# Kernel tuning notes

Hardware: AMD Instinct MI355X
Metric: run time of the kernel (lower is better)

The kernel has to match this reference:

```python
import jax, jax.numpy as jnp
import numpy as np

D_MODEL = 1024
SLOTS = 4096
LEVELS = 3
B, T = 4, 4096
TOP_K = 8  # k = min(8, slots)


def setup_inputs() -> dict:
    key = jax.random.key(0)
    ks = jax.random.split(key, 8)
    # xavier-uniform-ish scale for K/V
    lim_kv = np.sqrt(6.0 / (SLOTS + D_MODEL)).astype(np.float32)
    lim_w1 = np.sqrt(6.0 / (D_MODEL + D_MODEL // 2)).astype(np.float32)
    lim_w2 = np.sqrt(6.0 / (D_MODEL // 2 + LEVELS)).astype(np.float32)
    return {
        "q": jax.random.normal(ks[0], (B, T, D_MODEL), dtype=jnp.float32),
        "Ks": jax.random.uniform(ks[1], (LEVELS, SLOTS, D_MODEL), jnp.float32, -lim_kv, lim_kv),
        "Vs": jax.random.uniform(ks[2], (LEVELS, SLOTS, D_MODEL), jnp.float32, -lim_kv, lim_kv),
        "saliences": jnp.zeros((LEVELS, SLOTS), dtype=jnp.float32),
        "router_W1": jax.random.uniform(ks[3], (D_MODEL, D_MODEL // 2), jnp.float32, -lim_w1, lim_w1),
        "router_b1": jnp.zeros((D_MODEL // 2,), dtype=jnp.float32),
        "router_W2": jax.random.uniform(ks[4], (D_MODEL // 2, LEVELS), jnp.float32, -lim_w2, lim_w2),
        "router_b2": jnp.zeros((LEVELS,), dtype=jnp.float32),
    }


def reference(q, Ks, Vs, saliences, router_W1, router_b1, router_W2, router_b2):
    Bq, Tq, D = q.shape
    inv_sqrt_d = 1.0 / jnp.sqrt(jnp.asarray(D, dtype=q.dtype))

    # router: Linear -> ReLU -> Linear -> softmax over levels
    h = jax.nn.relu(q @ router_W1 + router_b1)
    route_weights = jax.nn.softmax(h @ router_W2 + router_b2, axis=-1)  # [B,T,L]

    def per_level(K, V, salience, level_w):
        # K,V: [S,D]; salience: [S]; level_w: [B,T]
        scores = jnp.einsum('btd,sd->bts', q, K) * inv_sqrt_d + salience  # [B,T,S]
        topk_scores, topk_idx = jax.lax.top_k(scores, TOP_K)  # [B,T,k]
        attn = jax.nn.softmax(topk_scores, axis=-1)  # [B,T,k]
        V_sel = V[topk_idx]  # [B,T,k,D] irregular gather
        read = jnp.einsum('btk,btkd->btd', attn, V_sel)  # [B,T,D]
        return read * level_w[..., None]

    # route_weights per level: [L,B,T]
    reads = jax.vmap(per_level, in_axes=(0, 0, 0, 2))(
        Ks, Vs, saliences, route_weights)  # [L,B,T,D]
    final_read = reads.sum(axis=0)
    return final_read
```

## Files before the change

### kernel.cpp

```cpp
#include <hip/hip_runtime.h>
#include <hip/hip_bf16.h>
#include <math.h>

#define D_MODEL 1024
#define SLOTS   4096
#define LEVELS  3
#define BT      16384
#define HDIM    512
#define NCAND   16
#define TOPK    8

#define QSCALE 25.0f
#define KSCALE 3700.0f
#define DELTA  2.5e-3f

typedef float  f32x4  __attribute__((ext_vector_type(4)));
typedef int    i32x4  __attribute__((ext_vector_type(4)));
typedef __bf16 bf16x8 __attribute__((ext_vector_type(8)));

__device__ __forceinline__ void gl_lds16(const void* g, void* l) {
  __builtin_amdgcn_global_load_lds((const __attribute__((address_space(1))) void*)g,
                                   (__attribute__((address_space(3))) void*)l, 16, 0, 0);
}

__device__ __forceinline__ unsigned short f2bf(float f) {
  union { float f; unsigned u; } v; v.f = f;
  unsigned r = (v.u + 0x7fffu + ((v.u >> 16) & 1u)) >> 16;
  return (unsigned short)r;
}
__device__ __forceinline__ float bf2f(unsigned short b) {
  union { unsigned u; float f; } v; v.u = ((unsigned)b) << 16; return v.f;
}
__device__ __forceinline__ int q_i8(float f, float scale) {
  float v = f * scale;
  v = fminf(fmaxf(v, -127.0f), 127.0f);
  return (int)rintf(v);
}
__device__ __forceinline__ unsigned umaxu(unsigned a, unsigned b) { return a > b ? a : b; }
__device__ __forceinline__ unsigned uminu(unsigned a, unsigned b) { return a < b ? a : b; }

__global__ __launch_bounds__(256) void conv_i8_kernel(const float* __restrict__ src,
                                                      char* __restrict__ dst, float scale) {
  int i = blockIdx.x * 256 + threadIdx.x;
  const float4* s = (const float4*)src + i * 4;
  int w[4];
#pragma unroll
  for (int g = 0; g < 4; ++g) {
    float4 v = s[g];
    int b0 = q_i8(v.x, scale) & 255, b1 = q_i8(v.y, scale) & 255;
    int b2 = q_i8(v.z, scale) & 255, b3 = q_i8(v.w, scale) & 255;
    w[g] = b0 | (b1 << 8) | (b2 << 16) | (b3 << 24);
  }
  ((int4*)dst)[i] = make_int4(w[0], w[1], w[2], w[3]);
}

__global__ __launch_bounds__(256) void conv_q_kernel(const float* __restrict__ q,
                                                     unsigned short* __restrict__ qh,
                                                     unsigned short* __restrict__ ql) {
  int i = blockIdx.x * 256 + threadIdx.x;
  float4 v = ((const float4*)q)[i];
  float vv[4] = {v.x, v.y, v.z, v.w};
  unsigned h[4], l[4];
#pragma unroll
  for (int e = 0; e < 4; ++e) {
    unsigned short hb = f2bf(vv[e]);
    h[e] = hb;
    l[e] = f2bf(vv[e] - bf2f(hb));
  }
  uint2 hp, lp;
  hp.x = h[0] | (h[1] << 16); hp.y = h[2] | (h[3] << 16);
  lp.x = l[0] | (l[1] << 16); lp.y = l[2] | (l[3] << 16);
  ((uint2*)qh)[i] = hp;
  ((uint2*)ql)[i] = lp;
}

__global__ __launch_bounds__(256) void conv_w1t_kernel(const float* __restrict__ W1,
                                                       unsigned short* __restrict__ Wh,
                                                       unsigned short* __restrict__ Wl) {
  int e = blockIdx.x * 256 + threadIdx.x;
  int k = e >> 9, n = e & 511;
  float f = W1[e];
  unsigned short hb = f2bf(f);
  Wh[(size_t)n * 1024 + k] = hb;
  Wl[(size_t)n * 1024 + k] = f2bf(f - bf2f(hb));
}

__global__ __launch_bounds__(256) void gemm_scores_i8_kernel(
    const char* __restrict__ A,
    const char* __restrict__ B,
    const float* __restrict__ sal,
    unsigned short* __restrict__ C) {
  __shared__ __align__(16) char As[128 * 64];
  __shared__ __align__(16) char Bs[128 * 64];
  const int tid = threadIdx.x;
  const int bx = blockIdx.x, by = blockIdx.y;
  const int lane = tid & 63, wave = tid >> 6;
  const int wm = wave >> 1, wn = wave & 1;

  const char* gA = A + (size_t)(by * 128 + (tid >> 2)) * 1024 + (tid & 3) * 16;
  const char* gB = B + (size_t)(bx * 128 + (tid >> 2)) * 1024 + (tid & 3) * 16;
  char* lA = As + tid * 16;
  char* lB = Bs + tid * 16;

  i32x4 acc[4][4] = {};

  for (int k0 = 0; k0 < 1024; k0 += 64) {
    __syncthreads();
    gl_lds16(gA + k0,             lA);
    gl_lds16(gA + 64 * 1024 + k0, lA + 64 * 64);
    gl_lds16(gB + k0,             lB);
    gl_lds16(gB + 64 * 1024 + k0, lB + 64 * 64);
    __syncthreads();

    const int fr = lane & 15, fk = (lane >> 4) * 16;
    i32x4 a[4], b[4];
#pragma unroll
    for (int i = 0; i < 4; ++i) a[i] = *(const i32x4*)(As + (wm * 64 + i * 16 + fr) * 64 + fk);
#pragma unroll
    for (int j = 0; j < 4; ++j) b[j] = *(const i32x4*)(Bs + (wn * 64 + j * 16 + fr) * 64 + fk);
#pragma unroll
    for (int i = 0; i < 4; ++i)
#pragma unroll
      for (int j = 0; j < 4; ++j)
        acc[i][j] = __builtin_amdgcn_mfma_i32_16x16x64_i8(a[i], b[j], acc[i][j], 0, 0, 0);
  }

  const float dq = 1.0f / (QSCALE * KSCALE * 32.0f);
  const int rr = (lane >> 4) * 4, cc = lane & 15;
#pragma unroll
  for (int i = 0; i < 4; ++i)
#pragma unroll
    for (int j = 0; j < 4; ++j) {
      int col = bx * 128 + wn * 64 + j * 16 + cc;
      float s = sal[col];
      int rowb = by * 128 + wm * 64 + i * 16 + rr;
#pragma unroll
      for (int r = 0; r < 4; ++r)
        C[(size_t)(rowb + r) * 4096 + col] = f2bf((float)acc[i][j][r] * dq + s);
    }
}

__global__ __launch_bounds__(256) void gemm_router_kernel(
    const unsigned short* __restrict__ Ah, const unsigned short* __restrict__ Al,
    const unsigned short* __restrict__ Bh, const unsigned short* __restrict__ Bl,
    const float* __restrict__ b1, float* __restrict__ H) {
  __shared__ __align__(16) unsigned short Ash[128 * 32], Asl[128 * 32];
  __shared__ __align__(16) unsigned short Bsh[128 * 32], Bsl[128 * 32];
  const int tid = threadIdx.x;
  const int bx = blockIdx.x, by = blockIdx.y;
  const int lane = tid & 63, wave = tid >> 6;
  const int wm = wave >> 1, wn = wave & 1;

  const int s_row = wave * 16 + (lane >> 2);
  const int s_c8  = (lane & 3) * 8;
  const unsigned short* gAh = Ah + (size_t)(by * 128 + s_row) * 1024 + s_c8;
  const unsigned short* gAl = Al + (size_t)(by * 128 + s_row) * 1024 + s_c8;
  const unsigned short* gBh = Bh + (size_t)(bx * 128 + s_row) * 1024 + s_c8;
  const unsigned short* gBl = Bl + (size_t)(bx * 128 + s_row) * 1024 + s_c8;
  unsigned short* lAh = Ash + s_row * 32 + s_c8;
  unsigned short* lAl = Asl + s_row * 32 + s_c8;
  unsigned short* lBh = Bsh + s_row * 32 + s_c8;
  unsigned short* lBl = Bsl + s_row * 32 + s_c8;

  f32x4 acc[4][4] = {};

  for (int k0 = 0; k0 < 1024; k0 += 32) {
    __syncthreads();
    gl_lds16(gAh + k0,             lAh);
    gl_lds16(gAh + 64 * 1024 + k0, lAh + 64 * 32);
    gl_lds16(gAl + k0,             lAl);
    gl_lds16(gAl + 64 * 1024 + k0, lAl + 64 * 32);
    gl_lds16(gBh + k0,             lBh);
    gl_lds16(gBh + 64 * 1024 + k0, lBh + 64 * 32);
    gl_lds16(gBl + k0,             lBl);
    gl_lds16(gBl + 64 * 1024 + k0, lBl + 64 * 32);
    __syncthreads();

    const int fr = lane & 15, fk = (lane >> 4) * 8;
    bf16x8 ah[4], al[4], bh[4], bl[4];
#pragma unroll
    for (int i = 0; i < 4; ++i) {
      int off = (wm * 64 + i * 16 + fr) * 32 + fk;
      ah[i] = *(const bf16x8*)(Ash + off);
      al[i] = *(const bf16x8*)(Asl + off);
    }
#pragma unroll
    for (int j = 0; j < 4; ++j) {
      int off = (wn * 64 + j * 16 + fr) * 32 + fk;
      bh[j] = *(const bf16x8*)(Bsh + off);
      bl[j] = *(const bf16x8*)(Bsl + off);
    }
#pragma unroll
    for (int i = 0; i < 4; ++i)
#pragma unroll
      for (int j = 0; j < 4; ++j) {
        acc[i][j] = __builtin_amdgcn_mfma_f32_16x16x32_bf16(ah[i], bh[j], acc[i][j], 0, 0, 0);
        acc[i][j] = __builtin_amdgcn_mfma_f32_16x16x32_bf16(ah[i], bl[j], acc[i][j], 0, 0, 0);
        acc[i][j] = __builtin_amdgcn_mfma_f32_16x16x32_bf16(al[i], bh[j], acc[i][j], 0, 0, 0);
      }
  }

  const int rr = (lane >> 4) * 4, cc = lane & 15;
#pragma unroll
  for (int i = 0; i < 4; ++i)
#pragma unroll
    for (int j = 0; j < 4; ++j) {
      int col = bx * 128 + wn * 64 + j * 16 + cc;
      float bias = b1[col];
      int rowb = by * 128 + wm * 64 + i * 16 + rr;
#pragma unroll
      for (int r = 0; r < 4; ++r) {
        float v = acc[i][j][r] + bias;
        H[(size_t)(rowb + r) * HDIM + col] = v > 0.0f ? v : 0.0f;
      }
    }
}

__global__ __launch_bounds__(256) void router_head_kernel(
    const float* __restrict__ H, const float* __restrict__ W2,
    const float* __restrict__ b2, float* __restrict__ route_w) {
  int wave = threadIdx.x >> 6, lane = threadIdx.x & 63;
  int row = blockIdx.x * 4 + wave;
  float a0 = 0.f, a1 = 0.f, a2 = 0.f;
#pragma unroll
  for (int k = 0; k < 8; ++k) {
    int d = k * 64 + lane;
    float hv = H[(size_t)row * HDIM + d];
    a0 += hv * W2[d * 3 + 0];
    a1 += hv * W2[d * 3 + 1];
    a2 += hv * W2[d * 3 + 2];
  }
#pragma unroll
  for (int m = 1; m < 64; m <<= 1) {
    a0 += __shfl_xor(a0, m); a1 += __shfl_xor(a1, m); a2 += __shfl_xor(a2, m);
  }
  if (lane == 0) {
    float l0 = a0 + b2[0], l1 = a1 + b2[1], l2 = a2 + b2[2];
    float mx = fmaxf(l0, fmaxf(l1, l2));
    float e0 = expf(l0 - mx), e1 = expf(l1 - mx), e2 = expf(l2 - mx);
    float inv = 1.0f / (e0 + e1 + e2);
    route_w[(size_t)row * 3 + 0] = e0 * inv;
    route_w[(size_t)row * 3 + 1] = e1 * inv;
    route_w[(size_t)row * 3 + 2] = e2 * inv;
  }
}

template<bool FILTER>
__device__ __forceinline__ void top4_build(const uint4 (&v)[8], unsigned lane8, unsigned bound,
                                           unsigned &t0, unsigned &t1, unsigned &t2, unsigned &t3) {
  t0 = t1 = t2 = t3 = 0u;
#pragma unroll
  for (int i = 0; i < 8; ++i) {
    unsigned wds[4] = {v[i].x, v[i].y, v[i].z, v[i].w};
#pragma unroll
    for (int g = 0; g < 4; ++g) {
      unsigned w = wds[g];
      unsigned s = w & 0x80008000u;
      unsigned key2 = (w ^ 0x80008000u) ^ (s - (s >> 15));
      unsigned pb = lane8 + (unsigned)(i * 512 + g * 2);
      unsigned kA = (key2 << 16) | pb;
      unsigned kB = (key2 & 0xFFFF0000u) | (pb + 1u);
      if (FILTER) {
        if (kA >= bound) kA = 0u;
        if (kB >= bound) kB = 0u;
      }
      unsigned x, y, z;
      x = uminu(t0, kA); t0 = umaxu(t0, kA);
      y = uminu(t1, x);  t1 = umaxu(t1, x);
      z = uminu(t2, y);  t2 = umaxu(t2, y);
      t3 = umaxu(t3, z);
      x = uminu(t0, kB); t0 = umaxu(t0, kB);
      y = uminu(t1, x);  t1 = umaxu(t1, x);
      z = uminu(t2, y);  t2 = umaxu(t2, y);
      t3 = umaxu(t3, z);
    }
  }
}

__global__ __launch_bounds__(256) void select_kernel(
    const unsigned short* __restrict__ S,
    int2* __restrict__ cand2, int c0, int level) {
  int wave = threadIdx.x >> 6, lane = threadIdx.x & 63;
  int rlocal = blockIdx.x * 4 + wave;
  const uint4* row = (const uint4*)(S + (size_t)rlocal * 4096);

  uint4 v[8];
#pragma unroll
  for (int i = 0; i < 8; ++i) v[i] = row[i * 64 + lane];

  const unsigned lane8 = (unsigned)lane * 8u;
  unsigned t0, t1, t2, t3;
  top4_build<false>(v, lane8, 0u, t0, t1, t2, t3);

  unsigned myres = 0u;
#pragma clang loop unroll(disable)
  for (int r = 0; r < NCAND; ++r) {
    unsigned g = t0;
#pragma unroll
    for (int m = 1; m < 64; m <<= 1) {
      unsigned o = (unsigned)__shfl_xor((int)g, m);
      g = umaxu(g, o);
    }
    if (t0 == g) {
      t0 = t1; t1 = t2; t2 = t3; t3 = 0u;
      if (t0 == 0u)
        top4_build<true>(v, lane8, g, t0, t1, t2, t3);
    }
    if (lane == r) myres = g;
  }

  size_t base = ((size_t)(c0 + rlocal) * 3 + level) * NCAND;
  if (lane < NCAND) {
    unsigned k16 = myres >> 16;
    unsigned ob = k16 ^ ((k16 & 0x8000u) ? 0x8000u : 0xFFFFu);
    cand2[base + lane] = make_int2((int)(myres & 0xFFFFu),
                                   __float_as_int(bf2f((unsigned short)ob)));
  }
}

__global__ __launch_bounds__(256) void rescore_kernel(
    const float* __restrict__ q, const float* __restrict__ Kl,
    const float* __restrict__ sal, const float* __restrict__ route_w,
    const int2* __restrict__ cand2, int level, int c0,
    int* __restrict__ sel_idx, float* __restrict__ sel_w) {
  int wave = threadIdx.x >> 6, lane = threadIdx.x & 63;
  int row = c0 + blockIdx.x * 4 + wave;

  float av[NCAND]; int idx[NCAND];
  {
    size_t cb = ((size_t)row * 3 + level) * NCAND;
#pragma unroll
    for (int c = 0; c < NCAND; ++c) {
      int2 pr = cand2[cb + c];
      idx[c] = pr.x; av[c] = __int_as_float(pr.y);
    }
  }

  int cin_mask = 0, amb_mask = 0;
#pragma unroll
  for (int i = 0; i < NCAND; ++i) {
    int cnt_hi = 0, cnt_lo = 0;
#pragma unroll
    for (int j = 0; j < NCAND; ++j) {
      cnt_hi += (av[j] > av[i] + DELTA) ? 1 : 0;
      cnt_lo += (j != i && av[j] > av[i] - DELTA) ? 1 : 0;
    }
    if (cnt_hi >= TOPK) {  }
    else if (cnt_lo <= TOPK - 1) cin_mask |= (1 << i);
    else amb_mask |= (1 << i);
  }
  int need = TOPK - __popc((unsigned)cin_mask);

  double ex[NCAND];
  if (need > 0 && amb_mask) {
    float qr[16];
    const float4* qp = (const float4*)(q + (size_t)row * 1024) + lane * 4;
#pragma unroll
    for (int m4 = 0; m4 < 4; ++m4) {
      float4 tv = qp[m4];
      qr[m4 * 4 + 0] = tv.x; qr[m4 * 4 + 1] = tv.y;
      qr[m4 * 4 + 2] = tv.z; qr[m4 * 4 + 3] = tv.w;
    }
    for (int c = 0; c < NCAND; ++c) {
      if (!((amb_mask >> c) & 1)) continue;
      int sx = idx[c];
      const float4* kr = (const float4*)(Kl + (size_t)sx * 1024) + lane * 4;
      double acc = 0.0;
#pragma unroll
      for (int m4 = 0; m4 < 4; ++m4) {
        float4 kv = kr[m4];
        acc = fma((double)qr[m4 * 4 + 0], (double)kv.x, acc);
        acc = fma((double)qr[m4 * 4 + 1], (double)kv.y, acc);
        acc = fma((double)qr[m4 * 4 + 2], (double)kv.z, acc);
        acc = fma((double)qr[m4 * 4 + 3], (double)kv.w, acc);
      }
#pragma unroll
      for (int m = 1; m < 64; m <<= 1) acc += __shfl_xor(acc, m);
      ex[c] = acc * 0.03125 + (double)sal[sx];
    }
  }

  int cs[TOPK]; int ns = 0;
#pragma unroll
  for (int i = 0; i < NCAND; ++i)
    if ((cin_mask >> i) & 1) cs[ns++] = i;
  unsigned rem = (unsigned)amb_mask;
  for (int p = 0; p < need; ++p) {
    double bs = -1e300; int bc = -1;
    for (int c = 0; c < NCAND; ++c)
      if ((rem >> c) & 1)
        if (ex[c] > bs) { bs = ex[c]; bc = c; }
    rem &= ~(1u << bc);
    cs[ns++] = bc;
  }

  float mx = -INFINITY;
#pragma unroll
  for (int k = 0; k < TOPK; ++k) mx = fmaxf(mx, av[cs[k]]);
  float ew[TOPK], sum = 0.f;
#pragma unroll
  for (int k = 0; k < TOPK; ++k) { ew[k] = expf(av[cs[k]] - mx); sum += ew[k]; }
  float rw = route_w[(size_t)row * 3 + level] / sum;
  if (lane == 0) {
    size_t base = ((size_t)row * 3 + level) * TOPK;
#pragma unroll
    for (int k = 0; k < TOPK; ++k) {
      sel_idx[base + k] = idx[cs[k]];
      sel_w[base + k]  = ew[k] * rw;
    }
  }
}

__global__ __launch_bounds__(256) void final_kernel(
    const float* __restrict__ Vs, const int* __restrict__ sel_idx,
    const float* __restrict__ sel_w, float* __restrict__ out) {
  __shared__ float wv[24];
  __shared__ int   widx[24];
  int row = blockIdx.x, t = threadIdx.x;
  if (t < 24) {
    int l = t >> 3, j = t & 7;
    size_t base = ((size_t)row * 3 + l) * TOPK + j;
    wv[t]   = sel_w[base];
    widx[t] = l * SLOTS + sel_idx[base];
  }
  __syncthreads();
  float4 acc = {0.f, 0.f, 0.f, 0.f};
  for (int i = 0; i < 24; ++i) {
    float w = wv[i];
    float4 v = ((const float4*)(Vs + (size_t)widx[i] * 1024))[t];
    acc.x += w * v.x; acc.y += w * v.y; acc.z += w * v.z; acc.w += w * v.w;
  }
  ((float4*)(out + (size_t)row * 1024))[t] = acc;
}

extern "C" void kernel_launch(void* const* d_in, const int* in_sizes, int n_in,
                              void* d_out, int out_size, void* d_ws, size_t ws_size,
                              hipStream_t stream) {
  const float* q   = (const float*)d_in[0];
  const float* Ks  = (const float*)d_in[1];
  const float* Vs  = (const float*)d_in[2];
  const float* sal = (const float*)d_in[3];
  const float* W1  = (const float*)d_in[4];
  const float* b1  = (const float*)d_in[5];
  const float* W2  = (const float*)d_in[6];
  const float* b2  = (const float*)d_in[7];
  float* out = (float*)d_out;
  (void)in_sizes; (void)n_in; (void)out_size;

  char* p = (char*)d_ws;
  auto alloc = [&](size_t bytes) -> char* {
    char* r = p; p += (bytes + 255) & ~(size_t)255; return r;
  };
  char*  q8    = alloc((size_t)BT * 1024);
  char*  K8    = alloc((size_t)LEVELS * SLOTS * 1024);
  float* route = (float*)alloc((size_t)BT * 3 * 4);
  int2*  cand2 = (int2*)alloc((size_t)BT * 3 * NCAND * 8);
  int*   s_idx = (int*)alloc((size_t)BT * 3 * TOPK * 4);
  float* s_w   = (float*)alloc((size_t)BT * 3 * TOPK * 4);
  size_t fixed = (size_t)(p - (char*)d_ws);

  char* ali = p;
  unsigned short* qh   = (unsigned short*)alloc((size_t)BT * 1024 * 2);
  unsigned short* ql   = (unsigned short*)alloc((size_t)BT * 1024 * 2);
  unsigned short* W1Th = (unsigned short*)alloc((size_t)HDIM * 1024 * 2);
  unsigned short* W1Tl = (unsigned short*)alloc((size_t)HDIM * 1024 * 2);
  float*          h    = (float*)alloc((size_t)BT * HDIM * 4);
  size_t router_bytes = (size_t)(p - ali);

  unsigned short* scores = (unsigned short*)ali;
  int chunk = 2048;
  const int opts[4] = {16384, 8192, 4096, 2048};
  for (int i = 0; i < 4; ++i) {
    size_t scores_b = (size_t)opts[i] * SLOTS * 2;
    size_t need = fixed + (scores_b > router_bytes ? scores_b : router_bytes);
    if (need <= ws_size) { chunk = opts[i]; break; }
  }

  conv_i8_kernel<<<(BT * 1024 / 16) / 256, 256, 0, stream>>>(q, q8, QSCALE);
  conv_i8_kernel<<<(LEVELS * SLOTS * 1024 / 16) / 256, 256, 0, stream>>>(Ks, K8, KSCALE);
  conv_q_kernel<<<(BT * 1024 / 4) / 256, 256, 0, stream>>>(q, qh, ql);
  conv_w1t_kernel<<<(1024 * HDIM) / 256, 256, 0, stream>>>(W1, W1Th, W1Tl);

  gemm_router_kernel<<<dim3(HDIM / 128, BT / 128), 256, 0, stream>>>(qh, ql, W1Th, W1Tl, b1, h);
  router_head_kernel<<<BT / 4, 256, 0, stream>>>(h, W2, b2, route);

  for (int level = 0; level < LEVELS; ++level) {
    const char*  K8L  = K8 + (size_t)level * SLOTS * 1024;
    const float* salL = sal + (size_t)level * SLOTS;
    const float* KsL  = Ks + (size_t)level * SLOTS * 1024;
    for (int c0 = 0; c0 < BT; c0 += chunk) {
      gemm_scores_i8_kernel<<<dim3(SLOTS / 128, chunk / 128), 256, 0, stream>>>(
          q8 + (size_t)c0 * 1024, K8L, salL, scores);
      select_kernel<<<chunk / 4, 256, 0, stream>>>(scores, cand2, c0, level);
      rescore_kernel<<<chunk / 4, 256, 0, stream>>>(q, KsL, salL, route, cand2, level, c0, s_idx, s_w);
    }
  }

  final_kernel<<<BT, 256, 0, stream>>>(Vs, s_idx, s_w, out);
}
```

Before: 1.194 ms.

## Fuse q conversions, drop q low-part in router GEMM, gather V in fp16

The int8 and bf16 conversions of q are merged into one kernel that reads q once. The router GEMM drops the low-order bf16 part of q, cutting a third of its MFMAs plus the matching LDS and global traffic, at some cost in router precision. V is converted once to fp16 so the final gather reads half the bytes. The extra conversion pass over V costs bandwidth and adds rounding error to the output.

Measured after the change: 1.068 ms. 10.5% less time.

```diff
diff --git a/kernel.cpp b/kernel.cpp
--- a/kernel.cpp
+++ b/kernel.cpp
@@ -14,9 +14,10 @@
 #define KSCALE 3700.0f
 #define DELTA  2.5e-3f
 
-typedef float  f32x4  __attribute__((ext_vector_type(4)));
-typedef int    i32x4  __attribute__((ext_vector_type(4)));
-typedef __bf16 bf16x8 __attribute__((ext_vector_type(8)));
+typedef float    f32x4  __attribute__((ext_vector_type(4)));
+typedef int      i32x4  __attribute__((ext_vector_type(4)));
+typedef __bf16   bf16x8 __attribute__((ext_vector_type(8)));
+typedef _Float16 f16x8  __attribute__((ext_vector_type(8)));
 
 __device__ __forceinline__ void gl_lds16(const void* g, void* l) {
   __builtin_amdgcn_global_load_lds((const __attribute__((address_space(1))) void*)g,
@@ -54,24 +55,25 @@
   ((int4*)dst)[i] = make_int4(w[0], w[1], w[2], w[3]);
 }
 
-__global__ __launch_bounds__(256) void conv_q_kernel(const float* __restrict__ q,
-                                                     unsigned short* __restrict__ qh,
-                                                     unsigned short* __restrict__ ql) {
+__global__ __launch_bounds__(256) void conv_q8h_kernel(const float* __restrict__ q,
+                                                       char* __restrict__ q8,
+                                                       unsigned short* __restrict__ qh) {
   int i = blockIdx.x * 256 + threadIdx.x;
-  float4 v = ((const float4*)q)[i];
-  float vv[4] = {v.x, v.y, v.z, v.w};
-  unsigned h[4], l[4];
-#pragma unroll
-  for (int e = 0; e < 4; ++e) {
-    unsigned short hb = f2bf(vv[e]);
-    h[e] = hb;
-    l[e] = f2bf(vv[e] - bf2f(hb));
-  }
-  uint2 hp, lp;
-  hp.x = h[0] | (h[1] << 16); hp.y = h[2] | (h[3] << 16);
-  lp.x = l[0] | (l[1] << 16); lp.y = l[2] | (l[3] << 16);
-  ((uint2*)qh)[i] = hp;
-  ((uint2*)ql)[i] = lp;
+  const float4* s = (const float4*)q + i * 4;
+  int w[4]; unsigned hh[8];
+#pragma unroll
+  for (int g = 0; g < 4; ++g) {
+    float4 v = s[g];
+    int b0 = q_i8(v.x, QSCALE) & 255, b1 = q_i8(v.y, QSCALE) & 255;
+    int b2 = q_i8(v.z, QSCALE) & 255, b3 = q_i8(v.w, QSCALE) & 255;
+    w[g] = b0 | (b1 << 8) | (b2 << 16) | (b3 << 24);
+    hh[g * 2 + 0] = (unsigned)f2bf(v.x) | ((unsigned)f2bf(v.y) << 16);
+    hh[g * 2 + 1] = (unsigned)f2bf(v.z) | ((unsigned)f2bf(v.w) << 16);
+  }
+  ((int4*)q8)[i] = make_int4(w[0], w[1], w[2], w[3]);
+  uint4* qp = (uint4*)qh + i * 2;
+  qp[0] = make_uint4(hh[0], hh[1], hh[2], hh[3]);
+  qp[1] = make_uint4(hh[4], hh[5], hh[6], hh[7]);
 }
 
 __global__ __launch_bounds__(256) void conv_w1t_kernel(const float* __restrict__ W1,
@@ -83,6 +85,17 @@
   unsigned short hb = f2bf(f);
   Wh[(size_t)n * 1024 + k] = hb;
   Wl[(size_t)n * 1024 + k] = f2bf(f - bf2f(hb));
+}
+
+__global__ __launch_bounds__(256) void conv_v16_kernel(const float* __restrict__ Vs,
+                                                       _Float16* __restrict__ V16) {
+  int i = blockIdx.x * 256 + threadIdx.x;
+  const float4* s = (const float4*)Vs + i * 2;
+  float4 a = s[0], b = s[1];
+  f16x8 o;
+  o[0] = (_Float16)a.x; o[1] = (_Float16)a.y; o[2] = (_Float16)a.z; o[3] = (_Float16)a.w;
+  o[4] = (_Float16)b.x; o[5] = (_Float16)b.y; o[6] = (_Float16)b.z; o[7] = (_Float16)b.w;
+  ((f16x8*)V16)[i] = o;
 }
 
 __global__ __launch_bounds__(256) void gemm_scores_i8_kernel(
@@ -141,10 +154,10 @@
 }
 
 __global__ __launch_bounds__(256) void gemm_router_kernel(
-    const unsigned short* __restrict__ Ah, const unsigned short* __restrict__ Al,
+    const unsigned short* __restrict__ Ah,
     const unsigned short* __restrict__ Bh, const unsigned short* __restrict__ Bl,
     const float* __restrict__ b1, float* __restrict__ H) {
-  __shared__ __align__(16) unsigned short Ash[128 * 32], Asl[128 * 32];
+  __shared__ __align__(16) unsigned short Ash[128 * 32];
   __shared__ __align__(16) unsigned short Bsh[128 * 32], Bsl[128 * 32];
   const int tid = threadIdx.x;
   const int bx = blockIdx.x, by = blockIdx.y;
@@ -154,11 +167,9 @@
   const int s_row = wave * 16 + (lane >> 2);
   const int s_c8  = (lane & 3) * 8;
   const unsigned short* gAh = Ah + (size_t)(by * 128 + s_row) * 1024 + s_c8;
-  const unsigned short* gAl = Al + (size_t)(by * 128 + s_row) * 1024 + s_c8;
   const unsigned short* gBh = Bh + (size_t)(bx * 128 + s_row) * 1024 + s_c8;
   const unsigned short* gBl = Bl + (size_t)(bx * 128 + s_row) * 1024 + s_c8;
   unsigned short* lAh = Ash + s_row * 32 + s_c8;
-  unsigned short* lAl = Asl + s_row * 32 + s_c8;
   unsigned short* lBh = Bsh + s_row * 32 + s_c8;
   unsigned short* lBl = Bsl + s_row * 32 + s_c8;
 
@@ -168,8 +179,6 @@
     __syncthreads();
     gl_lds16(gAh + k0,             lAh);
     gl_lds16(gAh + 64 * 1024 + k0, lAh + 64 * 32);
-    gl_lds16(gAl + k0,             lAl);
-    gl_lds16(gAl + 64 * 1024 + k0, lAl + 64 * 32);
     gl_lds16(gBh + k0,             lBh);
     gl_lds16(gBh + 64 * 1024 + k0, lBh + 64 * 32);
     gl_lds16(gBl + k0,             lBl);
@@ -177,12 +186,11 @@
     __syncthreads();
 
     const int fr = lane & 15, fk = (lane >> 4) * 8;
-    bf16x8 ah[4], al[4], bh[4], bl[4];
+    bf16x8 ah[4], bh[4], bl[4];
 #pragma unroll
     for (int i = 0; i < 4; ++i) {
       int off = (wm * 64 + i * 16 + fr) * 32 + fk;
       ah[i] = *(const bf16x8*)(Ash + off);
-      al[i] = *(const bf16x8*)(Asl + off);
     }
 #pragma unroll
     for (int j = 0; j < 4; ++j) {
@@ -196,7 +204,6 @@
       for (int j = 0; j < 4; ++j) {
         acc[i][j] = __builtin_amdgcn_mfma_f32_16x16x32_bf16(ah[i], bh[j], acc[i][j], 0, 0, 0);
         acc[i][j] = __builtin_amdgcn_mfma_f32_16x16x32_bf16(ah[i], bl[j], acc[i][j], 0, 0, 0);
-        acc[i][j] = __builtin_amdgcn_mfma_f32_16x16x32_bf16(al[i], bh[j], acc[i][j], 0, 0, 0);
       }
   }
 
@@ -411,8 +418,8 @@
   }
 }
 
-__global__ __launch_bounds__(256) void final_kernel(
-    const float* __restrict__ Vs, const int* __restrict__ sel_idx,
+__global__ __launch_bounds__(128) void final_kernel(
+    const _Float16* __restrict__ V16, const int* __restrict__ sel_idx,
     const float* __restrict__ sel_w, float* __restrict__ out) {
   __shared__ float wv[24];
   __shared__ int   widx[24];
@@ -424,13 +431,16 @@
     widx[t] = l * SLOTS + sel_idx[base];
   }
   __syncthreads();
-  float4 acc = {0.f, 0.f, 0.f, 0.f};
+  float acc[8] = {0.f, 0.f, 0.f, 0.f, 0.f, 0.f, 0.f, 0.f};
   for (int i = 0; i < 24; ++i) {
     float w = wv[i];
-    float4 v = ((const float4*)(Vs + (size_t)widx[i] * 1024))[t];
-    acc.x += w * v.x; acc.y += w * v.y; acc.z += w * v.z; acc.w += w * v.w;
-  }
-  ((float4*)(out + (size_t)row * 1024))[t] = acc;
+    f16x8 v = *(const f16x8*)(V16 + (size_t)widx[i] * 1024 + t * 8);
+#pragma unroll
+    for (int e = 0; e < 8; ++e) acc[e] += w * (float)v[e];
+  }
+  float4* op = (float4*)(out + (size_t)row * 1024) + t * 2;
+  op[0] = make_float4(acc[0], acc[1], acc[2], acc[3]);
+  op[1] = make_float4(acc[4], acc[5], acc[6], acc[7]);
 }
 
 extern "C" void kernel_launch(void* const* d_in, const int* in_sizes, int n_in,
@@ -451,17 +461,17 @@
   auto alloc = [&](size_t bytes) -> char* {
     char* r = p; p += (bytes + 255) & ~(size_t)255; return r;
   };
-  char*  q8    = alloc((size_t)BT * 1024);
-  char*  K8    = alloc((size_t)LEVELS * SLOTS * 1024);
-  float* route = (float*)alloc((size_t)BT * 3 * 4);
-  int2*  cand2 = (int2*)alloc((size_t)BT * 3 * NCAND * 8);
-  int*   s_idx = (int*)alloc((size_t)BT * 3 * TOPK * 4);
-  float* s_w   = (float*)alloc((size_t)BT * 3 * TOPK * 4);
+  char*      q8    = alloc((size_t)BT * 1024);
+  char*      K8    = alloc((size_t)LEVELS * SLOTS * 1024);
+  _Float16*  V16   = (_Float16*)alloc((size_t)LEVELS * SLOTS * 1024 * 2);
+  float*     route = (float*)alloc((size_t)BT * 3 * 4);
+  int2*      cand2 = (int2*)alloc((size_t)BT * 3 * NCAND * 8);
+  int*       s_idx = (int*)alloc((size_t)BT * 3 * TOPK * 4);
+  float*     s_w   = (float*)alloc((size_t)BT * 3 * TOPK * 4);
   size_t fixed = (size_t)(p - (char*)d_ws);
 
   char* ali = p;
   unsigned short* qh   = (unsigned short*)alloc((size_t)BT * 1024 * 2);
-  unsigned short* ql   = (unsigned short*)alloc((size_t)BT * 1024 * 2);
   unsigned short* W1Th = (unsigned short*)alloc((size_t)HDIM * 1024 * 2);
   unsigned short* W1Tl = (unsigned short*)alloc((size_t)HDIM * 1024 * 2);
   float*          h    = (float*)alloc((size_t)BT * HDIM * 4);
@@ -476,12 +486,12 @@
     if (need <= ws_size) { chunk = opts[i]; break; }
   }
 
-  conv_i8_kernel<<<(BT * 1024 / 16) / 256, 256, 0, stream>>>(q, q8, QSCALE);
+  conv_q8h_kernel<<<(BT * 1024 / 16) / 256, 256, 0, stream>>>(q, q8, qh);
   conv_i8_kernel<<<(LEVELS * SLOTS * 1024 / 16) / 256, 256, 0, stream>>>(Ks, K8, KSCALE);
-  conv_q_kernel<<<(BT * 1024 / 4) / 256, 256, 0, stream>>>(q, qh, ql);
+  conv_v16_kernel<<<(LEVELS * SLOTS * 1024 / 8) / 256, 256, 0, stream>>>(Vs, V16);
   conv_w1t_kernel<<<(1024 * HDIM) / 256, 256, 0, stream>>>(W1, W1Th, W1Tl);
 
-  gemm_router_kernel<<<dim3(HDIM / 128, BT / 128), 256, 0, stream>>>(qh, ql, W1Th, W1Tl, b1, h);
+  gemm_router_kernel<<<dim3(HDIM / 128, BT / 128), 256, 0, stream>>>(qh, W1Th, W1Tl, b1, h);
   router_head_kernel<<<BT / 4, 256, 0, stream>>>(h, W2, b2, route);
 
   for (int level = 0; level < LEVELS; ++level) {
@@ -496,5 +506,5 @@
     }
   }
 
-  final_kernel<<<BT, 256, 0, stream>>>(Vs, s_idx, s_w, out);
-}
+  final_kernel<<<BT, 128, 0, stream>>>(V16, s_idx, s_w, out);
+}
```
